# Performance work log

Hardware: AMD Instinct MI355X
Metric: run time of the kernel (lower is better)

## Reference

```python
import jax, jax.numpy as jnp
import numpy as np

BIG = 1e9      # infinity sentinel used by the CUDA kernels
THRESH = 1e8   # 'min_val >= 1e8 -> invalid' cutoff
MAX_LEN = 512  # init kwarg max_length
BANDWIDTH = 0.2


def _dist(X, Y):
    # pairwise squared-euclidean: D[b,i,j] = sum_d (X[b,i,d]-Y[b,j,d])^2
    diff = X[:, :, None, :] - Y[:, None, :, :]  # [B,N,M,d]
    return jnp.sum(diff * diff, axis=-1)        # [B,N,M]


def _ldtw_dp(D, max_len, bandwidth):
    """Band-limited length-constrained DTW DP.
    Returns (min_vals[B], choices[max_len,B,N,M] int8, best_k[B]).
    choices[t] holds the step-(k=t+1) decisions at interior cells (i-1, j-1)."""
    B, N, M = D.shape
    ii = np.arange(1, N + 1)[:, None]
    jj = np.arange(1, M + 1)[None, :]
    band_bad = jnp.asarray((np.abs(ii - jj) > bandwidth * max(N, M)) & (bandwidth > 0))  # [N,M] static

    # prev_cost padded [B, N+2, M+2]; only (0,0) starts at 0, everything else BIG.
    prev0 = jnp.full((B, N + 2, M + 2), BIG, jnp.float32).at[:, 0, 0].set(0.0)

    def step(prev, _):
        # candidates for interior cells (i in 1..N, j in 1..M)
        cand = jnp.stack(
            [prev[:, 0:N, 0:M],       # diag  (choice 0)
             prev[:, 0:N, 1:M + 1],   # vert  (choice 1)
             prev[:, 1:N + 1, 0:M]],  # hori  (choice 2)
            axis=0)                    # [3,B,N,M]
        min_val = cand.min(axis=0)
        # argmin returns first minimum -> matches strict-less update order (diag,vert,hori)
        choice = jnp.argmin(cand, axis=0).astype(jnp.int8)
        valid = min_val < THRESH
        cost = jnp.where(band_bad[None] | ~valid, BIG, min_val + D)
        ch = jnp.where(valid & ~band_bad[None], choice, jnp.int8(-1))
        curr = jnp.full_like(prev, BIG).at[:, 1:N + 1, 1:M + 1].set(cost)
        return curr, (cost[:, N - 1, M - 1], ch)

    _, (final_costs, choices) = jax.lax.scan(step, prev0, None, length=max_len)
    # final_costs[t] is the cost of a length-(t+1) path ending at (N,M)
    mvl = max(N, M)
    valid_costs = final_costs[mvl - 1:]            # k in [mvl, max_len]
    min_vals = valid_costs.min(axis=0)             # [B]
    best_k = jnp.argmin(valid_costs, axis=0) + mvl # [B] (unused in fwd)
    return min_vals, choices, best_k


def setup_inputs() -> dict:
    key = jax.random.key(0)
    k1, k2 = jax.random.split(key)
    X = jax.random.normal(k1, (16, 256, 64), jnp.float32)
    Y = jax.random.normal(k2, (16, 256, 64), jnp.float32)
    return {"X": X, "Y": Y}


def reference(X, Y):
    D = _dist(X, Y)
    min_vals, _, _ = _ldtw_dp(D, MAX_LEN, BANDWIDTH)
    # original module returns (min_vals, None); the None carries no information
    return min_vals
```

## Files before the change

### kernel.cpp

```cpp
#include <hip/hip_runtime.h>

#define BIGV 1e9f
#define NPT 256

__device__ __forceinline__ int imin_of(int s){
    int a = s - 255; if (a < 0) a = 0;
    int c = s - 50;  c = (c > 0) ? (c >> 1) : 0;
    return (a > c) ? a : c;
}
__device__ __forceinline__ int imax_of(int s){
    int a = (s < 255) ? s : 255;
    int c = (s + 51) >> 1;
    return (a < c) ? a : c;
}

__device__ __forceinline__ float dpp_shr1(float x){
    return __int_as_float(__builtin_amdgcn_update_dpp(
        __float_as_int(BIGV), __float_as_int(x), 0x138 , 0xF, 0xF, false));
}
__device__ __forceinline__ float dpp_shl1(float x){
    return __int_as_float(__builtin_amdgcn_update_dpp(
        __float_as_int(BIGV), __float_as_int(x), 0x130 , 0xF, 0xF, false));
}

__device__ __forceinline__ float min3f(float a, float b, float c){
    float r;
    asm("v_min3_f32 %0, %1, %2, %3" : "=v"(r) : "v"(a), "v"(b), "v"(c));
    return r;
}

__global__ __launch_bounds__(256, 1) void ldtw_dist(const float* __restrict__ X,
                                                    const float* __restrict__ Y,
                                                    float* __restrict__ Df)
{
    __shared__ float4 Xs[80*17];
    __shared__ float4 Ys[80*17];
    __shared__ float nX[80], nY[80];
    __shared__ float Band[32*65];
    const int b  = blockIdx.x & 15;
    const int c  = blockIdx.x >> 4;
    const int s0 = c << 5;
    const int s1 = (s0 + 31 > 510) ? 510 : (s0 + 31);
    const int ilo = imin_of(s0), ihi = imax_of(s1);
    const int jlo = s0 - imax_of(s0), jhi = s1 - imin_of(s1);
    const int nx = ihi - ilo + 1, ny = jhi - jlo + 1;
    const int t = threadIdx.x;
    const float4* Xb = (const float4*)(X + (size_t)b * NPT * 64);
    const float4* Yb = (const float4*)(Y + (size_t)b * NPT * 64);

    for (int idx = t; idx < nx * 16; idx += 256){
        int r = idx >> 4, k = idx & 15;
        Xs[r*17 + k] = Xb[(ilo + r)*16 + k];
    }
    for (int idx = t; idx < ny * 16; idx += 256){
        int r = idx >> 4, k = idx & 15;
        Ys[r*17 + k] = Yb[(jlo + r)*16 + k];
    }
    __syncthreads();

    for (int r = t; r < nx + ny; r += 256){
        const float4* row = (r < nx) ? (Xs + r*17) : (Ys + (r - nx)*17);
        float acc = 0.f;
        #pragma unroll
        for (int k = 0; k < 16; ++k){
            float4 v = row[k];
            acc += v.x*v.x + v.y*v.y + v.z*v.z + v.w*v.w;
        }
        if (r < nx) nX[r] = acc; else nY[r - nx] = acc;
    }
    __syncthreads();

    {
        const int ti = t >> 4;
        const int tj = t & 15;
        float acc[5][5];
        #pragma unroll
        for (int u = 0; u < 5; ++u)
            #pragma unroll
            for (int v = 0; v < 5; ++v) acc[u][v] = 0.f;

        #pragma unroll 4
        for (int k = 0; k < 16; ++k){
            float4 xa[5], ya[5];
            #pragma unroll
            for (int u = 0; u < 5; ++u){
                xa[u] = Xs[(ti + u*16)*17 + k];
                ya[u] = Ys[(tj + u*16)*17 + k];
            }
            #pragma unroll
            for (int u = 0; u < 5; ++u)
                #pragma unroll
                for (int v = 0; v < 5; ++v)
                    acc[u][v] += xa[u].x*ya[v].x + xa[u].y*ya[v].y
                               + xa[u].z*ya[v].z + xa[u].w*ya[v].w;
        }

        #pragma unroll
        for (int u = 0; u < 5; ++u){
            #pragma unroll
            for (int v = 0; v < 5; ++v){
                const int iloc = ti + u*16, jloc = tj + v*16;
                const int i = ilo + iloc, j = jlo + jloc;
                const int s = i + j;
                if (s >= s0 && s <= s1){
                    const int im = imin_of(s), ix = imax_of(s);
                    if (i >= im && i <= ix)
                        Band[(s - s0)*65 + (i - im)] =
                            nX[iloc] + nY[jloc] - 2.f*acc[u][v];
                }
            }
        }
    }
    __syncthreads();

    float4* Df4 = (float4*)Df;
    const size_t rowbase4 = ((size_t)(b * 512 + s0)) << 6;
    for (int slot = t; slot < 32*64; slot += 256){
        const int sd = slot >> 6, q = slot & 63;
        const int s  = s0 + sd;
        float4 v = make_float4(BIGV, BIGV, BIGV, BIGV);
        if (s <= 510){
            const int im = imin_of(s), ix = imax_of(s);
            const int i0 = q << 2;
            if (i0 + 0 >= im && i0 + 0 <= ix) v.x = Band[sd*65 + (i0 + 0 - im)];
            if (i0 + 1 >= im && i0 + 1 <= ix) v.y = Band[sd*65 + (i0 + 1 - im)];
            if (i0 + 2 >= im && i0 + 2 <= ix) v.z = Band[sd*65 + (i0 + 2 - im)];
            if (i0 + 3 >= im && i0 + 3 <= ix) v.w = Band[sd*65 + (i0 + 3 - im)];
        }
        Df4[rowbase4 + ((size_t)sd << 6) + q] = v;
    }
}

__global__ __launch_bounds__(64) void ldtw_dp(const float* __restrict__ Df,
                                              float* __restrict__ out)
{
    const int b = blockIdx.x;
    const int L = threadIdx.x;
    const float4* base = (const float4*)Df + ((size_t)b << 15) + L;

    float p0, p1, p2, p3, q0, q1, q2, q3;
    float d00 = Df[(size_t)b << 17];
    p0 = (L == 0) ? d00 : BIGV; p1 = BIGV; p2 = BIGV; p3 = BIGV;
    q0 = BIGV; q1 = BIGV; q2 = BIGV; q3 = BIGV;

#define LOADG(Bk, g) { \
    const float4* r0_ = base + (size_t)(((g) << 3) + 1) * 64; \
    const float4* r1_ = r0_ + 256; \
    Bk##0 = r0_[0];   Bk##1 = r0_[64];  Bk##2 = r0_[128]; Bk##3 = r0_[192]; \
    Bk##4 = r1_[0];   Bk##5 = r1_[64];  Bk##6 = r1_[128]; Bk##7 = r1_[192]; }

#define STEP_PQ(V) { \
    float s1_ = dpp_shr1(p3), s2_ = dpp_shr1(q3); \
    float n0 = min3f(s1_, p0, s2_) + (V).x; \
    float n1 = min3f(p0, p1, q0) + (V).y; \
    float n2 = min3f(p1, p2, q1) + (V).z; \
    float n3 = min3f(p2, p3, q2) + (V).w; \
    q0 = n0; q1 = n1; q2 = n2; q3 = n3; }
#define STEP_QP(V) { \
    float s1_ = dpp_shr1(q3), s2_ = dpp_shr1(p3); \
    float n0 = min3f(s1_, q0, s2_) + (V).x; \
    float n1 = min3f(q0, q1, p0) + (V).y; \
    float n2 = min3f(q1, q2, p1) + (V).z; \
    float n3 = min3f(q2, q3, p2) + (V).w; \
    p0 = n0; p1 = n1; p2 = n2; p3 = n3; }

#define GROUP8(Bk) \
    STEP_PQ(Bk##0) STEP_QP(Bk##1) STEP_PQ(Bk##2) STEP_QP(Bk##3) \
    STEP_PQ(Bk##4) STEP_QP(Bk##5) STEP_PQ(Bk##6) STEP_QP(Bk##7)

    float4 A0,A1,A2,A3,A4,A5,A6,A7;
    float4 B0,B1,B2,B3,B4,B5,B6,B7;
    float4 C0,C1,C2,C3,C4,C5,C6,C7;
    float4 E0,E1,E2,E3,E4,E5,E6,E7;
    LOADG(A, 0) LOADG(B, 1) LOADG(C, 2) LOADG(E, 3)
    for (int m = 0; m < 60; m += 4){
        GROUP8(A) LOADG(A, m + 4)
        GROUP8(B) LOADG(B, m + 5)
        GROUP8(C) LOADG(C, m + 6)
        GROUP8(E) LOADG(E, m + 7)
    }
    GROUP8(A)
    GROUP8(B)
    GROUP8(C)
    STEP_PQ(E0) STEP_QP(E1) STEP_PQ(E2) STEP_QP(E3) STEP_PQ(E4) STEP_QP(E5)

    if (L == 63) out[b] = p3;
#undef LOADG
#undef STEP_PQ
#undef STEP_QP
#undef GROUP8
}

__device__ __forceinline__ float cell_d(const float4* __restrict__ Xb,
                                        const float4* __restrict__ Yb,
                                        int i, int j)
{
    const float4* xr = Xb + i*16;
    const float4* yr = Yb + j*16;
    float acc = 0.f;
    #pragma unroll
    for (int k = 0; k < 16; ++k){
        float4 a = xr[k], bb = yr[k];
        float dx = a.x-bb.x, dy = a.y-bb.y, dz = a.z-bb.z, dw = a.w-bb.w;
        acc += dx*dx + dy*dy + dz*dz + dw*dw;
    }
    return acc;
}

__global__ __launch_bounds__(64) void ldtw_fused_fb(const float* __restrict__ X,
                                                    const float* __restrict__ Y,
                                                    float* __restrict__ out)
{
    const int b = blockIdx.x;
    const int l = threadIdx.x;
    const float4* Xb = (const float4*)(X + (size_t)b * NPT * 64);
    const float4* Yb = (const float4*)(Y + (size_t)b * NPT * 64);
    float prev1 = (l == 0) ? cell_d(Xb, Yb, 0, 0) : BIGV;
    float prev2 = BIGV;
    int base1 = 0, base2 = 0;
    for (int s = 1; s <= 510; ++s){
        const int im = imin_of(s);
        const int ix = imax_of(s);
        const int i  = im + l;
        const bool act = (i <= ix);
        const int ic = act ? i : ix;
        const int j  = s - ic;
        float Dv = cell_d(Xb, Yb, ic, j);
        const int d1 = im - base1, d2 = im - base2;
        float sr1 = dpp_shr1(prev1), sl1 = dpp_shl1(prev1);
        float sr2 = dpp_shr1(prev2), sl2 = dpp_shl1(prev2);
        float m1 = d1 ? fminf(prev1, sl1) : fminf(sr1, prev1);
        float vd = (d2 == 0) ? sr2 : ((d2 == 2) ? sl2 : prev2);
        float m3 = fminf(m1, vd);
        float cur = act ? (m3 + Dv) : BIGV;
        prev2 = prev1; base2 = base1;
        prev1 = cur;   base1 = im;
    }
    if (l == 0) out[b] = prev1;
}

extern "C" void kernel_launch(void* const* d_in, const int* in_sizes, int n_in,
                              void* d_out, int out_size, void* d_ws, size_t ws_size,
                              hipStream_t stream)
{
    const float* X = (const float*)d_in[0];
    const float* Y = (const float*)d_in[1];
    float* out = (float*)d_out;
    const int Bn = in_sizes[0] / (NPT * 64);
    const size_t need = (size_t)Bn * 512 * 256 * 4 + 65536;
    if (ws_size >= need && Bn == 16){
        float* Df = (float*)d_ws;
        hipLaunchKernelGGL(ldtw_dist, dim3(256),  dim3(256), 0, stream, X, Y, Df);
        hipLaunchKernelGGL(ldtw_dp,   dim3(Bn),   dim3(64),  0, stream, Df, out);
    } else {
        hipLaunchKernelGGL(ldtw_fused_fb, dim3(Bn), dim3(64), 0, stream, X, Y, out);
    }
}
```

Measured before the change: 32.77 us.

## Store band as sliding 64-wide window per diagonal, one cell per lane in DP

The distance kernel now writes only a 64-cell window per anti-diagonal, indexed by a per-group window offset, instead of the full 256-wide diagonal padded with BIG. The DP kernel shrinks from four cells per lane to one, shifting its p/q state left via DPP whenever the window offset advances between groups of eight diagonals. This cuts workspace traffic and DP arithmetic by about four times. In exchange it adds data-dependent shift loops, a deeper eight-group register prefetch, and a lower unroll factor in the Gram loop.

```diff
diff --git a/kernel.cpp b/kernel.cpp
--- a/kernel.cpp
+++ b/kernel.cpp
@@ -14,6 +14,14 @@
     return (a < c) ? a : c;
 }
 
+__device__ __forceinline__ int Wof(int g){
+    int w = imin_of(8*g + 1) - 1;
+    return (w < 0) ? 0 : ((w > 192) ? 192 : w);
+}
+__device__ __forceinline__ int wrow_of(int s){
+    return (s == 0) ? 0 : Wof((s - 1) >> 3);
+}
+
 __device__ __forceinline__ float dpp_shr1(float x){
     return __int_as_float(__builtin_amdgcn_update_dpp(
         __float_as_int(BIGV), __float_as_int(x), 0x138 , 0xF, 0xF, false));
@@ -31,7 +39,7 @@
 
 __global__ __launch_bounds__(256, 1) void ldtw_dist(const float* __restrict__ X,
                                                     const float* __restrict__ Y,
-                                                    float* __restrict__ Df)
+                                                    float* __restrict__ Dwin)
 {
     __shared__ float4 Xs[80*17];
     __shared__ float4 Ys[80*17];
@@ -79,7 +87,7 @@
             #pragma unroll
             for (int v = 0; v < 5; ++v) acc[u][v] = 0.f;
 
-        #pragma unroll 4
+        #pragma unroll 2
         for (int k = 0; k < 16; ++k){
             float4 xa[5], ya[5];
             #pragma unroll
@@ -113,82 +121,80 @@
     }
     __syncthreads();
 
-    float4* Df4 = (float4*)Df;
-    const size_t rowbase4 = ((size_t)(b * 512 + s0)) << 6;
+    const size_t rowbase = (size_t)(b * 512 + s0) * 64;
     for (int slot = t; slot < 32*64; slot += 256){
-        const int sd = slot >> 6, q = slot & 63;
+        const int sd = slot >> 6, l = slot & 63;
         const int s  = s0 + sd;
-        float4 v = make_float4(BIGV, BIGV, BIGV, BIGV);
+        float val = BIGV;
         if (s <= 510){
+            const int W = wrow_of(s);
+            const int i = W + l;
             const int im = imin_of(s), ix = imax_of(s);
-            const int i0 = q << 2;
-            if (i0 + 0 >= im && i0 + 0 <= ix) v.x = Band[sd*65 + (i0 + 0 - im)];
-            if (i0 + 1 >= im && i0 + 1 <= ix) v.y = Band[sd*65 + (i0 + 1 - im)];
-            if (i0 + 2 >= im && i0 + 2 <= ix) v.z = Band[sd*65 + (i0 + 2 - im)];
-            if (i0 + 3 >= im && i0 + 3 <= ix) v.w = Band[sd*65 + (i0 + 3 - im)];
-        }
-        Df4[rowbase4 + ((size_t)sd << 6) + q] = v;
-    }
-}
-
-__global__ __launch_bounds__(64) void ldtw_dp(const float* __restrict__ Df,
+            if (i >= im && i <= ix) val = Band[sd*65 + (i - im)];
+        }
+        Dwin[rowbase + (size_t)sd*64 + l] = val;
+    }
+}
+
+__global__ __launch_bounds__(64) void ldtw_dp(const float* __restrict__ Dw,
                                               float* __restrict__ out)
 {
     const int b = blockIdx.x;
-    const int L = threadIdx.x;
-    const float4* base = (const float4*)Df + ((size_t)b << 15) + L;
-
-    float p0, p1, p2, p3, q0, q1, q2, q3;
-    float d00 = Df[(size_t)b << 17];
-    p0 = (L == 0) ? d00 : BIGV; p1 = BIGV; p2 = BIGV; p3 = BIGV;
-    q0 = BIGV; q1 = BIGV; q2 = BIGV; q3 = BIGV;
+    const int l = threadIdx.x;
+    const float* base = Dw + (size_t)b * 512 * 64 + l;
+
+    float p = base[0];
+    float q = BIGV;
 
 #define LOADG(Bk, g) { \
-    const float4* r0_ = base + (size_t)(((g) << 3) + 1) * 64; \
-    const float4* r1_ = r0_ + 256; \
-    Bk##0 = r0_[0];   Bk##1 = r0_[64];  Bk##2 = r0_[128]; Bk##3 = r0_[192]; \
-    Bk##4 = r1_[0];   Bk##5 = r1_[64];  Bk##6 = r1_[128]; Bk##7 = r1_[192]; }
-
-#define STEP_PQ(V) { \
-    float s1_ = dpp_shr1(p3), s2_ = dpp_shr1(q3); \
-    float n0 = min3f(s1_, p0, s2_) + (V).x; \
-    float n1 = min3f(p0, p1, q0) + (V).y; \
-    float n2 = min3f(p1, p2, q1) + (V).z; \
-    float n3 = min3f(p2, p3, q2) + (V).w; \
-    q0 = n0; q1 = n1; q2 = n2; q3 = n3; }
-#define STEP_QP(V) { \
-    float s1_ = dpp_shr1(q3), s2_ = dpp_shr1(p3); \
-    float n0 = min3f(s1_, q0, s2_) + (V).x; \
-    float n1 = min3f(q0, q1, p0) + (V).y; \
-    float n2 = min3f(q1, q2, p1) + (V).z; \
-    float n3 = min3f(q2, q3, p2) + (V).w; \
-    p0 = n0; p1 = n1; p2 = n2; p3 = n3; }
-
-#define GROUP8(Bk) \
+    const float* bp_ = base + (size_t)(8*(g) + 1) * 64; \
+    Bk##0 = bp_[0];   Bk##1 = bp_[64];  Bk##2 = bp_[128]; Bk##3 = bp_[192]; \
+    Bk##4 = bp_[256]; Bk##5 = bp_[320]; Bk##6 = bp_[384]; Bk##7 = bp_[448]; }
+
+#define SHIFTG(g) { \
+    int d_ = Wof(g) - Wof((g) - 1); \
+    for (int k_ = 0; k_ < d_; ++k_){ p = dpp_shl1(p); q = dpp_shl1(q); } }
+
+#define STEP_PQ(w) q = min3f(dpp_shr1(p), p, dpp_shr1(q)) + (w);
+#define STEP_QP(w) p = min3f(dpp_shr1(q), q, dpp_shr1(p)) + (w);
+
+#define GROUPF(Bk, g) { SHIFTG(g) \
     STEP_PQ(Bk##0) STEP_QP(Bk##1) STEP_PQ(Bk##2) STEP_QP(Bk##3) \
-    STEP_PQ(Bk##4) STEP_QP(Bk##5) STEP_PQ(Bk##6) STEP_QP(Bk##7)
-
-    float4 A0,A1,A2,A3,A4,A5,A6,A7;
-    float4 B0,B1,B2,B3,B4,B5,B6,B7;
-    float4 C0,C1,C2,C3,C4,C5,C6,C7;
-    float4 E0,E1,E2,E3,E4,E5,E6,E7;
+    STEP_PQ(Bk##4) STEP_QP(Bk##5) STEP_PQ(Bk##6) STEP_QP(Bk##7) }
+
+    float A0,A1,A2,A3,A4,A5,A6,A7;
+    float B0,B1,B2,B3,B4,B5,B6,B7;
+    float C0,C1,C2,C3,C4,C5,C6,C7;
+    float E0,E1,E2,E3,E4,E5,E6,E7;
+    float F0,F1,F2,F3,F4,F5,F6,F7;
+    float G0,G1,G2,G3,G4,G5,G6,G7;
+    float H0,H1,H2,H3,H4,H5,H6,H7;
+    float K0,K1,K2,K3,K4,K5,K6,K7;
+
     LOADG(A, 0) LOADG(B, 1) LOADG(C, 2) LOADG(E, 3)
-    for (int m = 0; m < 60; m += 4){
-        GROUP8(A) LOADG(A, m + 4)
-        GROUP8(B) LOADG(B, m + 5)
-        GROUP8(C) LOADG(C, m + 6)
-        GROUP8(E) LOADG(E, m + 7)
-    }
-    GROUP8(A)
-    GROUP8(B)
-    GROUP8(C)
-    STEP_PQ(E0) STEP_QP(E1) STEP_PQ(E2) STEP_QP(E3) STEP_PQ(E4) STEP_QP(E5)
-
-    if (L == 63) out[b] = p3;
+    LOADG(F, 4) LOADG(G, 5) LOADG(H, 6) LOADG(K, 7)
+
+    for (int m = 0; m < 56; m += 8){
+        GROUPF(A, m + 0) LOADG(A, m + 8)
+        GROUPF(B, m + 1) LOADG(B, m + 9)
+        GROUPF(C, m + 2) LOADG(C, m + 10)
+        GROUPF(E, m + 3) LOADG(E, m + 11)
+        GROUPF(F, m + 4) LOADG(F, m + 12)
+        GROUPF(G, m + 5) LOADG(G, m + 13)
+        GROUPF(H, m + 6) LOADG(H, m + 14)
+        GROUPF(K, m + 7) LOADG(K, m + 15)
+    }
+    GROUPF(A, 56) GROUPF(B, 57) GROUPF(C, 58) GROUPF(E, 59)
+    GROUPF(F, 60) GROUPF(G, 61) GROUPF(H, 62)
+    SHIFTG(63)
+    STEP_PQ(K0) STEP_QP(K1) STEP_PQ(K2) STEP_QP(K3) STEP_PQ(K4) STEP_QP(K5)
+
+    if (l == 63) out[b] = p;
 #undef LOADG
+#undef SHIFTG
 #undef STEP_PQ
 #undef STEP_QP
-#undef GROUP8
+#undef GROUPF
 }
 
 __device__ __forceinline__ float cell_d(const float4* __restrict__ Xb,
@@ -247,11 +253,11 @@
     const float* Y = (const float*)d_in[1];
     float* out = (float*)d_out;
     const int Bn = in_sizes[0] / (NPT * 64);
-    const size_t need = (size_t)Bn * 512 * 256 * 4 + 65536;
+    const size_t need = (size_t)Bn * 512 * 64 * 4 + 65536;
     if (ws_size >= need && Bn == 16){
-        float* Df = (float*)d_ws;
-        hipLaunchKernelGGL(ldtw_dist, dim3(256),  dim3(256), 0, stream, X, Y, Df);
-        hipLaunchKernelGGL(ldtw_dp,   dim3(Bn),   dim3(64),  0, stream, Df, out);
+        float* Dwin = (float*)d_ws;
+        hipLaunchKernelGGL(ldtw_dist, dim3(256), dim3(256), 0, stream, X, Y, Dwin);
+        hipLaunchKernelGGL(ldtw_dp,   dim3(Bn),  dim3(64),  0, stream, Dwin, out);
     } else {
         hipLaunchKernelGGL(ldtw_fused_fb, dim3(Bn), dim3(64), 0, stream, X, Y, out);
     }
```

Result: faster. 31.82 us (-2.9%).
